# Performance work log

Hardware: AMD Instinct MI355X
Metric: run time of the kernel (lower is better)

## Reference

```python
import jax, jax.numpy as jnp
import numpy as np

DIM = 256
N_EMBED = 8192


def setup_inputs() -> dict:
    key = jax.random.key(0)
    k1, k2 = jax.random.split(key)
    x = jax.random.normal(k1, (16, 32, 32, DIM), dtype=jnp.float32)
    embed = jax.random.normal(k2, (DIM, N_EMBED), dtype=jnp.float32)
    return {"x": x, "embed": embed}


def reference(x, embed):
    """VQ-VAE quantizer forward (training mode): nearest-codebook lookup,
    straight-through quantize, commitment diff, and EMA stat accumulators.
    dist uses the mm-based squared-euclidean expansion (argmin is invariant
    to the sqrt in torch.cdist)."""
    dim, n_embed = embed.shape
    flat = x.reshape(-1, dim)  # [N, dim]
    dist = (
        jnp.sum(flat * flat, axis=1, keepdims=True)
        - 2.0 * (flat @ embed)
        + jnp.sum(embed * embed, axis=0, keepdims=True)
    )
    ind = jnp.argmin(dist, axis=1)  # [N]
    # embedding gather (embed_code): embed.T is [n_embed, dim]
    quantize = jnp.take(embed.T, ind, axis=0).reshape(x.shape)
    # EMA accumulation stats (training branch):
    # embed_onehot_sum[k] = count of tokens assigned to code k
    embed_onehot_sum = jax.ops.segment_sum(
        jnp.ones_like(ind, dtype=flat.dtype), ind, num_segments=n_embed
    )  # [n_embed]
    # embed_sum = flatten.T @ onehot == segment-sum of features per code
    embed_sum = jax.ops.segment_sum(flat, ind, num_segments=n_embed).T  # [dim, n_embed]
    diff = jnp.mean((jax.lax.stop_gradient(quantize) - x) ** 2)
    quantize_st = x + jax.lax.stop_gradient(quantize - x)
    embed_ind = ind.reshape(x.shape[:-1])
    return quantize_st, diff, embed_ind, embed_onehot_sum, embed_sum
```

## Files before the change

kernel.cpp:

```cpp
#include <hip/hip_runtime.h>

#define DIM   256
#define NE    8192
#define NTOK  16384

#define OFF_Q    0
#define OFF_DIFF 4194304
#define OFF_IND  4194305
#define OFF_OH   4210689
#define OFF_ES   4218881

#define NCAND 256
#define CAP   1024
#define CHUNK 64
#define DESC_MAX 8448

typedef __attribute__((ext_vector_type(8))) short short8;
typedef __attribute__((ext_vector_type(4))) float floatx4;

__device__ inline unsigned umin2(unsigned a, unsigned b) { return a < b ? a : b; }
__device__ inline unsigned umax2(unsigned a, unsigned b) { return a > b ? a : b; }

__device__ inline void gl_lds16(const void* g, void* l) {
    __builtin_amdgcn_global_load_lds(
        (const __attribute__((address_space(1))) unsigned int*)g,
        (__attribute__((address_space(3))) unsigned int*)l, 16, 0, 0);
}

__device__ inline unsigned short b16rn(float f) {
    unsigned u = __float_as_uint(f);
    unsigned r = (u + 0x7fffu + ((u >> 16) & 1u)) >> 16;
    return (unsigned short)r;
}

__global__ void convert_x_kernel(const float* __restrict__ x,
                                 unsigned short* __restrict__ Xbf) {
    int i = blockIdx.x * 256 + threadIdx.x;
    float4 v = ((const float4*)x)[i];
    ushort4 h;
    h.x = b16rn(v.x); h.y = b16rn(v.y); h.z = b16rn(v.z); h.w = b16rn(v.w);
    ((ushort4*)Xbf)[i] = h;
}

__global__ void convert_e_kernel(const float* __restrict__ embed,
                                 unsigned short* __restrict__ EbfT,
                                 float* __restrict__ embedT,
                                 float* __restrict__ e2,
                                 float* __restrict__ es2) {
    __shared__ __align__(16) float t2[32][DIM + 4];
    __shared__ float red[32][8];
    int c0 = blockIdx.x * 32;
    int tid = threadIdx.x;
    for (int t = 0; t < 32; ++t) {
        int i = t * 256 + tid;
        int d = i >> 5, c = i & 31;
        t2[c][d] = embed[(size_t)d * NE + c0 + c];
    }
    __syncthreads();
    for (int t = 0; t < 8; ++t) {
        int i = t * 256 + tid;
        int c = i >> 6, dq = i & 63;
        float4 v = *(const float4*)&t2[c][dq * 4];
        *(float4*)&embedT[(size_t)(c0 + c) * DIM + dq * 4] = v;
        ushort4 h;
        h.x = b16rn(-512.0f * v.x); h.y = b16rn(-512.0f * v.y);
        h.z = b16rn(-512.0f * v.z); h.w = b16rn(-512.0f * v.w);
        int C = c0 + c;
        int nb = C >> 7, n = C & 127;
        size_t off = (size_t)nb * 32768 + (size_t)(dq >> 3) * 4096 +
                     (size_t)((dq >> 1) & 3) * 1024 + (size_t)n * 8 + (dq & 1) * 4;
        *(ushort4*)&EbfT[off] = h;
    }
    {
        int c = tid >> 3, seg = tid & 7;
        float s = 0.f;
        for (int d = seg * 32; d < seg * 32 + 32; ++d)
            s = fmaf(t2[c][d], t2[c][d], s);
        red[c][seg] = s;
    }
    __syncthreads();
    if (tid < 32) {
        float s = 0.f;
        for (int j = 0; j < 8; ++j) s += red[tid][j];
        e2[c0 + tid] = s;
        es2[c0 + tid] = 256.0f * (512.0f + s);
    }
}

__global__ __launch_bounds__(256, 2) void dist_screen_kernel(
    const unsigned short* __restrict__ Xbf,
    const unsigned short* __restrict__ EbfT,
    const float* __restrict__ es2,
    unsigned int* __restrict__ cand) {
    __shared__ __align__(16) unsigned short Bs[2][16384];

    const int tid  = threadIdx.x;
    const int lane = tid & 63;
    const int wid  = tid >> 6;
    const int wm   = wid >> 1, wn = wid & 1;
    const int col  = lane & 15, quad = lane >> 4;
    const int nbg  = blockIdx.x;
    const int m0   = blockIdx.y * 128;

    short8 af[4][8];
#pragma unroll
    for (int mi = 0; mi < 4; ++mi) {
        const unsigned short* base =
            Xbf + (size_t)(m0 + wm * 64 + mi * 16 + col) * DIM + quad * 8;
#pragma unroll
        for (int kb = 0; kb < 8; ++kb)
            af[mi][kb] = *(const short8*)(base + kb * 32);
    }

    unsigned b1[16], b2[16];
#pragma unroll
    for (int i = 0; i < 16; ++i) { b1[i] = 0xFFFFFFFFu; b2[i] = 0xFFFFFFFFu; }

    const char* gbase = (const char*)EbfT + (size_t)nbg * 16 * 65536 +
                        (tid >> 6) * 2048 + (tid & 63) * 16;
    char* ldst0 = (char*)Bs + tid * 16;

#define STAGE(st, b)                                                          \
    {                                                                         \
        const char* s_ = gbase + ((st) >> 1) * 65536 + ((st) & 1) * 1024;     \
        char* d_ = ldst0 + (b) * 32768;                                       \
        _Pragma("unroll")                                                     \
        for (int i_ = 0; i_ < 8; ++i_)                                        \
            gl_lds16(s_ + i_ * 8192, d_ + i_ * 4096);                         \
    }

    STAGE(0, 0);
    __syncthreads();
    int cur = 0;
    const int n_a = wn * 32 + col;
    const int n_b = wn * 32 + 16 + col;

    for (int st = 0; st < 32; ++st) {
        if (st < 31) STAGE(st + 1, cur ^ 1);

        const int n0 = nbg * 2048 + st * 64;
        float e0 = es2[n0 + n_a];
        float e1 = es2[n0 + n_b];
        floatx4 acc[4][2];
#pragma unroll
        for (int mi = 0; mi < 4; ++mi) {
            acc[mi][0] = (floatx4)e0;
            acc[mi][1] = (floatx4)e1;
        }
        const unsigned short* B = &Bs[cur][0];
#pragma unroll
        for (int kb = 0; kb < 8; ++kb) {
            short8 bf0 = *(const short8*)&B[kb * 2048 + quad * 512 + n_a * 8];
            short8 bf1 = *(const short8*)&B[kb * 2048 + quad * 512 + n_b * 8];
#pragma unroll
            for (int mi = 0; mi < 4; ++mi) {
                acc[mi][0] = __builtin_amdgcn_mfma_f32_16x16x32_bf16(
                    af[mi][kb], bf0, acc[mi][0], 0, 0, 0);
                acc[mi][1] = __builtin_amdgcn_mfma_f32_16x16x32_bf16(
                    af[mi][kb], bf1, acc[mi][1], 0, 0, 0);
            }
        }
#pragma unroll
        for (int nj = 0; nj < 2; ++nj) {
            unsigned idxc = (unsigned)(n0 + wn * 32 + nj * 16 + col);
#pragma unroll
            for (int mi = 0; mi < 4; ++mi)
#pragma unroll
                for (int r = 0; r < 4; ++r) {
                    unsigned key = ((unsigned)acc[mi][nj][r] << 13) + idxc;
                    int s = mi * 4 + r;
                    unsigned lo = umin2(key, b1[s]);
                    unsigned hi = umax2(key, b1[s]);
                    b1[s] = lo;
                    b2[s] = umin2(hi, b2[s]);
                }
        }
        __syncthreads();
        cur ^= 1;
    }
#undef STAGE

#pragma unroll
    for (int mi = 0; mi < 4; ++mi)
#pragma unroll
        for (int r = 0; r < 4; ++r) {
            int token = m0 + wm * 64 + mi * 16 + quad * 4 + r;
            uint2 v; v.x = b1[mi * 4 + r]; v.y = b2[mi * 4 + r];
            *(uint2*)&cand[(size_t)token * NCAND + nbg * 64 + wn * 32 + col * 2] = v;
        }
}

__global__ __launch_bounds__(256) void finalize_kernel(
    const float* __restrict__ x, const float* __restrict__ embedT,
    const float* __restrict__ e2,
    const unsigned int* __restrict__ cand,
    float* __restrict__ out,
    unsigned int* __restrict__ cnt,
    unsigned short* __restrict__ slots,
    float* __restrict__ diffp) {
    __shared__ float partial[4];
    int tid = threadIdx.x, w = tid >> 6, lane = tid & 63;
    int l16 = lane & 15, grp = lane >> 4;
    int token = blockIdx.x * 4 + w;

    float4 xv = *(const float4*)&x[(size_t)token * DIM + lane * 4];
    float4 xg[4];
#pragma unroll
    for (int q = 0; q < 4; ++q)
        xg[q] = *(const float4*)&x[(size_t)token * DIM + q * 64 + l16 * 4];

    float x2 = xv.x * xv.x + xv.y * xv.y + xv.z * xv.z + xv.w * xv.w;
    uint4 c = *(const uint4*)&cand[(size_t)token * NCAND + lane * 4];
    unsigned g = umin2(umin2(c.x, c.y), umin2(c.z, c.w));
#pragma unroll
    for (int m = 1; m < 64; m <<= 1) {
        x2 += __shfl_xor(x2, m);
        g = umin2(g, (unsigned)__shfl_xor((int)g, m));
    }
    const unsigned thr = g + (384u << 13);

    float bd = 3.4e38f; int bk = 0x7fffffff;
    unsigned ca[4] = {c.x, c.y, c.z, c.w};
#pragma unroll
    for (int s = 0; s < 4; ++s) {
        unsigned long long mask = __ballot(ca[s] <= thr);
        while (mask) {
            int kk[4];
#pragma unroll
            for (int g2 = 0; g2 < 4; ++g2) {
                int l = mask ? (__ffsll(mask) - 1) : 0;
                int kv = __shfl((int)ca[s], l) & 8191;
                kk[g2] = mask ? kv : -1;
                mask &= mask - 1;
            }
            int myk = kk[grp];
            int kc = myk < 0 ? 0 : myk;
            const float* er = &embedT[(size_t)kc * DIM];
            float p = 0.f;
#pragma unroll
            for (int q = 0; q < 4; ++q) {
                float4 ev = *(const float4*)&er[q * 64 + l16 * 4];
                p = fmaf(xg[q].x, ev.x, p);
                p = fmaf(xg[q].y, ev.y, p);
                p = fmaf(xg[q].z, ev.z, p);
                p = fmaf(xg[q].w, ev.w, p);
            }
#pragma unroll
            for (int m = 1; m < 16; m <<= 1) p += __shfl_xor(p, m);
            float dg = (myk >= 0) ? (e2[kc] - 2.0f * p) : 3.4e38f;
#pragma unroll
            for (int g2 = 0; g2 < 4; ++g2) {
                float d2 = __shfl(dg, g2 * 16);
                int k2 = kk[g2];
                if (k2 >= 0 && (d2 < bd || (d2 == bd && k2 < bk))) {
                    bd = d2; bk = k2;
                }
            }
        }
    }
    float4 bq = *(const float4*)&embedT[(size_t)bk * DIM + lane * 4];
    *(float4*)&out[OFF_Q + (size_t)token * DIM + lane * 4] = bq;
    if (lane == 0) {
        out[OFF_IND + token] = (float)bk;
        unsigned pos = atomicAdd(&cnt[bk], 1u);
        if (pos < CAP) slots[(size_t)bk * CAP + pos] = (unsigned short)token;
        partial[w] = x2 + bd;
    }
    __syncthreads();
    if (tid == 0)
        diffp[blockIdx.x] =
            partial[0] + partial[1] + partial[2] + partial[3];
}

__global__ __launch_bounds__(256) void build_desc_kernel(
    const unsigned int* __restrict__ cnt,
    unsigned int* __restrict__ ndesc,
    unsigned int* __restrict__ desc) {
    int k = blockIdx.x * 256 + threadIdx.x;
    int lane = threadIdx.x & 63;
    unsigned n = cnt[k];
    unsigned nc = (n > CAP) ? 1u : (n + CHUNK - 1) >> 6;
    unsigned pfx = nc;
#pragma unroll
    for (int m = 1; m < 64; m <<= 1) {
        unsigned t = __shfl_up(pfx, m);
        if (lane >= m) pfx += t;
    }
    unsigned base = 0;
    if (lane == 63) base = atomicAdd(ndesc, pfx);
    base = __shfl(base, 63);
    unsigned off = base + pfx - nc;
    for (unsigned j = 0; j < nc; ++j)
        desc[off + j] = (unsigned)k | (j << 13);
}

__global__ __launch_bounds__(256) void embed_sum_kernel(
    const float* __restrict__ x,
    const unsigned int* __restrict__ cnt,
    const unsigned short* __restrict__ slots,
    const unsigned int* __restrict__ ndesc,
    const unsigned int* __restrict__ desc,
    const float* __restrict__ out_ind,
    float* __restrict__ esT) {
    int tid = threadIdx.x, w = tid >> 6, lane = tid & 63;
    unsigned wv = blockIdx.x * 4 + w;
    if (wv >= *ndesc) return;
    unsigned dsc = desc[wv];
    int k = dsc & 8191;
    int j = dsc >> 13;
    unsigned n = cnt[k];
    float ax = 0.f, ay = 0.f, az = 0.f, aw = 0.f;

    if (n > CAP) {
        for (int tok = 0; tok < NTOK; ++tok)
            if ((int)out_ind[tok] == k) {
                float4 v = *(const float4*)&x[(size_t)tok * DIM + lane * 4];
                ax += v.x; ay += v.y; az += v.z; aw += v.w;
            }
        *(float4*)&esT[(size_t)k * DIM + lane * 4] = make_float4(ax, ay, az, aw);
        return;
    }

    int base = j * CHUNK;
    int nt = (int)n - base; if (nt > CHUNK) nt = CHUNK;
    const unsigned short* sl = &slots[(size_t)k * CAP + base];
    for (int gr = 0; gr < CHUNK; gr += 8) {
        if (gr >= nt) break;
        uint4 sv = *(const uint4*)(sl + gr);
        unsigned id[8] = {sv.x & 0xffffu, sv.x >> 16, sv.y & 0xffffu, sv.y >> 16,
                          sv.z & 0xffffu, sv.z >> 16, sv.w & 0xffffu, sv.w >> 16};
        float4 v[8];
#pragma unroll
        for (int i = 0; i < 8; ++i) {
            unsigned tok = (gr + i < nt) ? id[i] : id[0];
            v[i] = *(const float4*)&x[(size_t)tok * DIM + lane * 4];
        }
#pragma unroll
        for (int i = 0; i < 8; ++i)
            if (gr + i < nt) { ax += v[i].x; ay += v[i].y; az += v[i].z; aw += v[i].w; }
    }

    float* dst = &esT[(size_t)k * DIM + lane * 4];
    if (n <= CHUNK) {
        *(float4*)dst = make_float4(ax, ay, az, aw);
    } else {
        atomicAdd(dst + 0, ax); atomicAdd(dst + 1, ay);
        atomicAdd(dst + 2, az); atomicAdd(dst + 3, aw);
    }
}

__global__ void es_out_kernel(const float* __restrict__ esT,
                              const unsigned int* __restrict__ cnt,
                              const float* __restrict__ diffp,
                              float* __restrict__ out) {
    __shared__ __align__(16) float t2[32][DIM + 4];
    __shared__ float rsum[256];
    int k0 = blockIdx.x * 32;
    int tid = threadIdx.x;
    for (int t = 0; t < 8; ++t) {
        int i = t * 256 + tid;
        int k = i >> 6, dq = i & 63;
        float4 v = ((const float4*)esT)[(size_t)(k0 + k) * 64 + dq];
        *(float4*)&t2[k][dq * 4] = v;
    }
    __syncthreads();
    for (int t = 0; t < 32; ++t) {
        int i = t * 256 + tid;
        int d = i >> 5, c = i & 31;
        out[OFF_ES + (size_t)d * NE + k0 + c] = t2[c][d];
    }
    if (tid < 32) out[OFF_OH + k0 + tid] = (float)cnt[k0 + tid];
    if (blockIdx.x == 0) {
        float s = 0.f;
        for (int i = tid; i < NTOK / 4; i += 256) s += diffp[i];
        rsum[tid] = s;
        __syncthreads();
        for (int st = 128; st > 0; st >>= 1) {
            if (tid < st) rsum[tid] += rsum[tid + st];
            __syncthreads();
        }
        if (tid == 0) out[OFF_DIFF] = rsum[0] * (1.0f / 4194304.0f);
    }
}

extern "C" void kernel_launch(void* const* d_in, const int* in_sizes, int n_in,
                              void* d_out, int out_size, void* d_ws, size_t ws_size,
                              hipStream_t stream) {
    const float* x     = (const float*)d_in[0];
    const float* embed = (const float*)d_in[1];
    float* out = (float*)d_out;

    char* p = (char*)d_ws;
    unsigned short* Xbf  = (unsigned short*)p;  p += (size_t)NTOK * DIM * 2;
    float* esT = (float*)Xbf;
    unsigned short* EbfT = (unsigned short*)p;  p += (size_t)NE * DIM * 2;
    float* embedT = (float*)p;                  p += (size_t)NE * DIM * 4;
    float* e2     = (float*)p;                  p += (size_t)NE * 4;
    float* es2    = (float*)p;                  p += (size_t)NE * 4;
    unsigned int* cand = (unsigned int*)p;      p += (size_t)NTOK * NCAND * 4;
    unsigned int* cnt  = (unsigned int*)p;      p += (size_t)NE * 4;
    unsigned int* ndesc = (unsigned int*)p;     p += 64;
    unsigned int* desc = (unsigned int*)p;      p += (size_t)(DESC_MAX + 64) * 4;
    float* diffp = (float*)p;                   p += (size_t)(NTOK / 4) * 4;
    unsigned short* slots = (unsigned short*)p; p += (size_t)NE * CAP * 2;

    hipMemsetAsync(cnt, 0, (size_t)NE * 4 + 64, stream);

    convert_x_kernel<<<(NTOK * DIM / 4) / 256, 256, 0, stream>>>(x, Xbf);
    convert_e_kernel<<<NE / 32, 256, 0, stream>>>(embed, EbfT, embedT, e2, es2);
    dist_screen_kernel<<<dim3(4, NTOK / 128), 256, 0, stream>>>(
        Xbf, EbfT, es2, cand);
    finalize_kernel<<<NTOK / 4, 256, 0, stream>>>(
        x, embedT, e2, cand, out, cnt, slots, diffp);
    build_desc_kernel<<<NE / 256, 256, 0, stream>>>(cnt, ndesc, desc);
    hipMemsetAsync(esT, 0, (size_t)NE * DIM * 4, stream);
    embed_sum_kernel<<<DESC_MAX / 4, 256, 0, stream>>>(
        x, cnt, slots, ndesc, desc, out + OFF_IND, esT);
    es_out_kernel<<<NE / 32, 256, 0, stream>>>(esT, cnt, diffp, out);
}
```

Before: 189.4 us.

## Software-pipeline MFMA and top-2 epilogue across stages with dual accumulators

The distance GEMM loop is unrolled by two with separate accumulator sets, so the top-2 key epilogue for one 64-code stage runs after the MFMAs of the next stage are issued. Overlapping the scalar min/max epilogue with matrix-core work is meant to hide epilogue latency. It doubles accumulator register use, which may raise VGPR pressure and lower occupancy.

```diff
diff --git a/kernel.cpp b/kernel.cpp
--- a/kernel.cpp
+++ b/kernel.cpp
@@ -129,56 +129,80 @@
             gl_lds16(s_ + i_ * 8192, d_ + i_ * 4096);                         \
     }
 
+    const int n_a = wn * 32 + col;
+    const int n_b = wn * 32 + 16 + col;
+
+#define INIT_ACC(A, st)                                                       \
+    {                                                                         \
+        const int n0_ = nbg * 2048 + (st) * 64;                               \
+        float e0_ = es2[n0_ + n_a];                                           \
+        float e1_ = es2[n0_ + n_b];                                           \
+        _Pragma("unroll")                                                     \
+        for (int mi_ = 0; mi_ < 4; ++mi_) {                                   \
+            A[mi_][0] = (floatx4)e0_; A[mi_][1] = (floatx4)e1_;               \
+        }                                                                     \
+    }
+
+#define MFMA_STEP(A, bufi)                                                    \
+    {                                                                         \
+        const unsigned short* B_ = &Bs[bufi][0];                              \
+        _Pragma("unroll")                                                     \
+        for (int kb_ = 0; kb_ < 8; ++kb_) {                                   \
+            short8 bf0_ = *(const short8*)&B_[kb_ * 2048 + quad * 512 + n_a * 8]; \
+            short8 bf1_ = *(const short8*)&B_[kb_ * 2048 + quad * 512 + n_b * 8]; \
+            _Pragma("unroll")                                                 \
+            for (int mi_ = 0; mi_ < 4; ++mi_) {                               \
+                A[mi_][0] = __builtin_amdgcn_mfma_f32_16x16x32_bf16(          \
+                    af[mi_][kb_], bf0_, A[mi_][0], 0, 0, 0);                  \
+                A[mi_][1] = __builtin_amdgcn_mfma_f32_16x16x32_bf16(          \
+                    af[mi_][kb_], bf1_, A[mi_][1], 0, 0, 0);                  \
+            }                                                                 \
+        }                                                                     \
+    }
+
+#define EPI_STEP(A, st)                                                       \
+    {                                                                         \
+        const int n0_ = nbg * 2048 + (st) * 64;                               \
+        _Pragma("unroll")                                                     \
+        for (int nj_ = 0; nj_ < 2; ++nj_) {                                   \
+            unsigned idxc_ = (unsigned)(n0_ + wn * 32 + nj_ * 16 + col);      \
+            _Pragma("unroll")                                                 \
+            for (int mi_ = 0; mi_ < 4; ++mi_)                                 \
+            _Pragma("unroll")                                                 \
+            for (int r_ = 0; r_ < 4; ++r_) {                                  \
+                unsigned key_ = ((unsigned)A[mi_][nj_][r_] << 13) + idxc_;    \
+                int s_ = mi_ * 4 + r_;                                        \
+                unsigned lo_ = umin2(key_, b1[s_]);                           \
+                unsigned hi_ = umax2(key_, b1[s_]);                           \
+                b1[s_] = lo_;                                                 \
+                b2[s_] = umin2(hi_, b2[s_]);     \
+            }                                                                 \
+        }                                                                     \
+    }
+
     STAGE(0, 0);
     __syncthreads();
-    int cur = 0;
-    const int n_a = wn * 32 + col;
-    const int n_b = wn * 32 + 16 + col;
-
-    for (int st = 0; st < 32; ++st) {
-        if (st < 31) STAGE(st + 1, cur ^ 1);
-
-        const int n0 = nbg * 2048 + st * 64;
-        float e0 = es2[n0 + n_a];
-        float e1 = es2[n0 + n_b];
-        floatx4 acc[4][2];
-#pragma unroll
-        for (int mi = 0; mi < 4; ++mi) {
-            acc[mi][0] = (floatx4)e0;
-            acc[mi][1] = (floatx4)e1;
-        }
-        const unsigned short* B = &Bs[cur][0];
-#pragma unroll
-        for (int kb = 0; kb < 8; ++kb) {
-            short8 bf0 = *(const short8*)&B[kb * 2048 + quad * 512 + n_a * 8];
-            short8 bf1 = *(const short8*)&B[kb * 2048 + quad * 512 + n_b * 8];
-#pragma unroll
-            for (int mi = 0; mi < 4; ++mi) {
-                acc[mi][0] = __builtin_amdgcn_mfma_f32_16x16x32_bf16(
-                    af[mi][kb], bf0, acc[mi][0], 0, 0, 0);
-                acc[mi][1] = __builtin_amdgcn_mfma_f32_16x16x32_bf16(
-                    af[mi][kb], bf1, acc[mi][1], 0, 0, 0);
-            }
-        }
-#pragma unroll
-        for (int nj = 0; nj < 2; ++nj) {
-            unsigned idxc = (unsigned)(n0 + wn * 32 + nj * 16 + col);
-#pragma unroll
-            for (int mi = 0; mi < 4; ++mi)
-#pragma unroll
-                for (int r = 0; r < 4; ++r) {
-                    unsigned key = ((unsigned)acc[mi][nj][r] << 13) + idxc;
-                    int s = mi * 4 + r;
-                    unsigned lo = umin2(key, b1[s]);
-                    unsigned hi = umax2(key, b1[s]);
-                    b1[s] = lo;
-                    b2[s] = umin2(hi, b2[s]);
-                }
-        }
+
+    floatx4 accA[4][2], accB[4][2];
+    for (int st2 = 0; st2 < 16; ++st2) {
+        const int stE = 2 * st2, stO = stE + 1;
+        STAGE(stO, 1);
+        INIT_ACC(accA, stE);
+        MFMA_STEP(accA, 0);
+        if (st2 > 0) EPI_STEP(accB, stE - 1);
         __syncthreads();
-        cur ^= 1;
-    }
+        if (stO < 31) STAGE(stO + 1, 0);
+        INIT_ACC(accB, stO);
+        MFMA_STEP(accB, 1);
+        EPI_STEP(accA, stE);
+        __syncthreads();
+    }
+    EPI_STEP(accB, 31);
+
 #undef STAGE
+#undef INIT_ACC
+#undef MFMA_STEP
+#undef EPI_STEP
 
 #pragma unroll
     for (int mi = 0; mi < 4; ++mi)
```

Result: slower. 200.4 us (+5.8%).
